# Kernel optimization log

Measured on AMD Instinct MI355X. Metric: run time of the kernel, lower is better.

## Reference

```python
import jax, jax.numpy as jnp
import numpy as np

N = 8192
D_IN = 512
HID = 1024
EMB = 64
N_EFF = 2
N_CLASSES = 16
MARGIN = 0.01


def setup_inputs() -> dict:
    key = jax.random.key(0)
    ks = jax.random.split(key, 10)
    data = jax.random.normal(ks[0], (N, D_IN), dtype=jnp.float32)
    labels = jax.random.randint(ks[1], (N,), 0, N_CLASSES).astype(jnp.float32)
    x = jnp.concatenate([labels[:, None], data], axis=1)  # [N, 1+D_IN]

    def lin(k, fan_in, fan_out):
        return jax.random.normal(k, (fan_in, fan_out), dtype=jnp.float32) / np.sqrt(fan_in)

    return {
        "x": x,
        "W1": lin(ks[2], D_IN, HID), "b1": jnp.zeros((HID,), jnp.float32),
        "W2": lin(ks[3], HID, EMB), "b2": jnp.zeros((EMB,), jnp.float32),
        "W3": lin(ks[4], EMB, HID), "b3": jnp.zeros((HID,), jnp.float32),
        "W4": lin(ks[5], HID, D_IN), "b4": jnp.zeros((D_IN,), jnp.float32),
    }


def reference(x, W1, b1, W2, b2, W3, b3, W4, b4):
    labels = x[:, 0]
    data = x[:, 1:]

    # encoder / decoder (tanh MLP autoencoder)
    embedding = jnp.tanh(data @ W1 + b1) @ W2 + b2          # [N, EMB]
    decoded = jnp.tanh(embedding @ W3 + b3) @ W4 + b4       # [N, D_IN]

    conserved = embedding[:, N_EFF:]                        # [N, C]
    n_conserved = conserved.shape[1]

    # labels.expand + unique(return_inverse) on row-replicated labels is
    # equivalent to comparing the labels directly.
    lbl = labels.astype(jnp.int32)
    Y = lbl[:, None] != lbl[None, :]                        # [N, N] bool

    # D_mean[i,j] = mean_d (c_i - c_j)^2, via Gram-matrix algebra (one pass,
    # no [N,N,C] intermediate).
    sq = jnp.sum(conserved * conserved, axis=1)             # [N]
    gram = conserved @ conserved.T                          # [N, N]
    D_mean = jnp.maximum(sq[:, None] + sq[None, :] - 2.0 * gram, 0.0) / n_conserved

    Yf = Y.astype(D_mean.dtype)
    n_diff = jnp.sum(Yf)
    C_sim = jnp.sum(Yf * D_mean) / (n_diff + 1.0)
    C_diff = jnp.sum((1.0 - Yf) * jnp.maximum(0.0, MARGIN - D_mean)) / (
        (D_mean.shape[0] * D_mean.shape[1] - n_diff) + 1.0)

    return decoded, C_sim, C_diff
```

## Files before the change

### kernel.cpp

```cpp
#include <hip/hip_runtime.h>
#include <stdint.h>

#define NROWS 8192
#define DIN   512
#define HIDN  1024
#define EMBN  64
#define NCONS 62
#define NCLS  16
#define MARGINF 0.01f
#define NREP  16

typedef unsigned short u16;
typedef __attribute__((ext_vector_type(8))) short short8;
typedef __attribute__((ext_vector_type(4))) float floatx4;

__device__ __forceinline__ u16 f32_to_bf16(float f) {
  union { float f; uint32_t u; } x; x.f = f;
  uint32_t u = x.u;
  uint32_t r = (u + 0x7FFFu + ((u >> 16) & 1u)) >> 16;
  return (u16)r;
}

__device__ __forceinline__ float bf16_to_f32(u16 h) {
  union { uint32_t u; float f; } x; x.u = (uint32_t)h << 16;
  return x.f;
}

__device__ __forceinline__ float fast_tanh(float x) {
  float xc = fminf(fmaxf(x, -10.f), 10.f);
  float e = __expf(2.f * xc);
  return (e - 1.f) * __builtin_amdgcn_rcpf(e + 1.f);
}

__device__ __forceinline__ void load_lds16(const u16* g, u16* l) {
  __builtin_amdgcn_global_load_lds(
      (const __attribute__((address_space(1))) void*)g,
      (__attribute__((address_space(3))) void*)l, 16, 0, 0);
}

__device__ __forceinline__ void pack_tile(const float* __restrict__ W,
                                          u16* __restrict__ Wp,
                                          int N, int KU, int t, int lane)
{
  const int r = lane >> 2, slot = lane & 3;
  const int c = slot ^ ((r >> 1) & 3);
  const int nt = t / KU, ku = t - nt * KU;
  const int n = nt * 16 + r;
  const int kb = ku * 32 + c * 8;
  short8 v;
#pragma unroll
  for (int j = 0; j < 8; ++j) v[j] = (short)f32_to_bf16(W[(size_t)(kb + j) * N + n]);
  *(short8*)(Wp + ((size_t)t * 64 + lane) * 8) = v;
}

__global__ __launch_bounds__(256)
void prep_all(const float* __restrict__ x,
              const float* __restrict__ W1, const float* __restrict__ W2,
              const float* __restrict__ W3, const float* __restrict__ W4,
              u16* __restrict__ A0p, u16* __restrict__ W1p,
              u16* __restrict__ W2p, u16* __restrict__ W3p,
              u16* __restrict__ W4p, float* __restrict__ slab,
              int* __restrict__ labels, int* __restrict__ hist32)
{
  __shared__ int hh[NCLS];
  const int b = blockIdx.x;
  const int tid = threadIdx.x;
  const int tl = tid >> 6, lane = tid & 63;
  if (b < 2048) {
    if (b < 32) {
      if (tid < NCLS) hh[tid] = 0;
      const int row = b * 256 + tid;
      const int lab = (int)x[(size_t)row * 513];
      labels[row] = lab;
      __syncthreads();
      atomicAdd(&hh[lab], 1);
      __syncthreads();
      if (tid < NCLS) hist32[b * NCLS + tid] = hh[tid];
    }
    const int t = b * 4 + tl;
    const int rt = t >> 4, ku = t & 15;
    const int r = lane & 15, q = lane >> 4;
    const float* src = x + (size_t)(rt * 16 + r) * 513 + 1 + ku * 32 + q * 8;
    short8 v;
#pragma unroll
    for (int j = 0; j < 8; ++j) v[j] = (short)f32_to_bf16(src[j]);
    *(short8*)(A0p + ((size_t)t * 64 + lane) * 8) = v;
  } else if (b < 2304) {
    pack_tile(W1, W1p, 1024, 16, (b - 2048) * 4 + tl, lane);
  } else if (b < 2336) {
    pack_tile(W2, W2p, 64, 32, (b - 2304) * 4 + tl, lane);
  } else if (b < 2368) {
    pack_tile(W3, W3p, 1024, 2, (b - 2336) * 4 + tl, lane);
  } else if (b < 2624) {
    pack_tile(W4, W4p, 512, 32, (b - 2368) * 4 + tl, lane);
  } else {
    float* dst = slab + (size_t)(b - 2624) * 4096;
    for (int i = tid; i < 4096; i += 256) dst[i] = 0.f;
  }
}

__global__ __launch_bounds__(256)
void gemm12(const u16* __restrict__ A0p, const u16* __restrict__ W1p,
            const float* __restrict__ b1, const u16* __restrict__ W2p,
            float* __restrict__ Ef4,
            const int* __restrict__ labels, const int* __restrict__ hist32,
            int* __restrict__ offs, int* __restrict__ counts,
            int* __restrict__ idx)
{
  __shared__ u16 lB[2][16 * 512];
  __shared__ u16 Hc[4][64 * 66];
  __shared__ int colsum[NCLS], preblk[NCLS], scur[NCLS];

  const int tid = threadIdx.x, wave = tid >> 6, lane = tid & 63;

  if (blockIdx.x >= 128) {
    const int sb = (blockIdx.x - 128) * 4 + blockIdx.y;
    if (tid < NCLS) {
      int s = 0, p = 0;
      for (int b2 = 0; b2 < 32; ++b2) {
        const int h = hist32[b2 * NCLS + tid];
        s += h;
        if (b2 < sb * 2) p += h;
      }
      colsum[tid] = s;
      preblk[tid] = p;
    }
    __syncthreads();
    if (tid < NCLS) {
      int o = 0;
      for (int c = 0; c < tid; ++c) o += colsum[c];
      scur[tid] = o + preblk[tid];
      if (sb == 0) {
        counts[tid] = colsum[tid];
        offs[tid] = o;
        if (tid == NCLS - 1) offs[NCLS] = o + colsum[NCLS - 1];
      }
    }
    __syncthreads();
    for (int i = tid; i < 512; i += 256) {
      const int row = sb * 512 + i;
      const int p = atomicAdd(&scur[labels[row]], 1);
      idx[p] = row;
    }
    return;
  }

  const int quad = lane >> 4, l15 = lane & 15;
  const int wm = wave >> 1, wn = wave & 1;
  const int xslot = (l15 >> 1) & 3;
  const int m0 = blockIdx.x * 64;
  const int g = blockIdx.y;

  floatx4 Hacc[4][2][2];
#pragma unroll
  for (int c = 0; c < 4; ++c)
#pragma unroll
    for (int i = 0; i < 2; ++i)
#pragma unroll
      for (int j = 0; j < 2; ++j) Hacc[c][i][j] = (floatx4){0.f, 0.f, 0.f, 0.f};

#pragma unroll
  for (int u = 0; u < 4; ++u) {
    const int jt = wave + u * 4;
    load_lds16(W1p + (size_t)((g * 16 + jt) * 16) * 512 + lane * 8, lB[0] + jt * 512);
  }
  __syncthreads();

  for (int s = 0; s < 16; ++s) {
    const int p = s & 1;
    if (s < 15) {
#pragma unroll
      for (int u = 0; u < 4; ++u) {
        const int jt = wave + u * 4;
        load_lds16(W1p + (size_t)((g * 16 + jt) * 16 + s + 1) * 512 + lane * 8,
                   lB[1 - p] + jt * 512);
      }
    }
    short8 af[2];
#pragma unroll
    for (int i = 0; i < 2; ++i)
      af[i] = *(const short8*)(A0p +
               (size_t)((blockIdx.x * 4 + wm * 2 + i) * 16 + s) * 512 + lane * 8);
#pragma unroll
    for (int c = 0; c < 4; ++c)
#pragma unroll
      for (int j = 0; j < 2; ++j) {
        const short8 bf = *(const short8*)(lB[p] + (c * 4 + wn * 2 + j) * 512
                              + l15 * 32 + ((quad ^ xslot) << 3));
#pragma unroll
        for (int i = 0; i < 2; ++i)
          Hacc[c][i][j] = __builtin_amdgcn_mfma_f32_16x16x32_bf16(af[i], bf, Hacc[c][i][j], 0, 0, 0);
      }
    __syncthreads();
  }

  u16* lW2 = &lB[0][0];
#pragma unroll
  for (int u = 0; u < 8; ++u) {
    const int t = wave * 8 + u;
    load_lds16(W2p + (size_t)((t >> 3) * 32 + g * 8 + (t & 7)) * 512 + lane * 8,
               lW2 + t * 512);
  }
#pragma unroll
  for (int c = 0; c < 4; ++c)
#pragma unroll
    for (int j = 0; j < 2; ++j) {
      const int col = wn * 32 + j * 16 + l15;
      const float bv = b1[g * 256 + c * 64 + col];
#pragma unroll
      for (int i = 0; i < 2; ++i)
#pragma unroll
        for (int r = 0; r < 4; ++r)
          Hc[c][(wm * 32 + i * 16 + quad * 4 + r) * 66 + col] =
              f32_to_bf16(fast_tanh(Hacc[c][i][j][r] + bv));
    }
  __syncthreads();

  floatx4 Eacc[2][2];
#pragma unroll
  for (int i = 0; i < 2; ++i)
#pragma unroll
    for (int j = 0; j < 2; ++j) Eacc[i][j] = (floatx4){0.f, 0.f, 0.f, 0.f};

#pragma unroll
  for (int es = 0; es < 8; ++es) {
    const int cc = es >> 1, hh2 = es & 1;
    short8 af2[2];
#pragma unroll
    for (int i = 0; i < 2; ++i)
      af2[i] = *(const short8*)(Hc[cc] + (wm * 32 + i * 16 + l15) * 66 + hh2 * 32 + quad * 8);
#pragma unroll
    for (int j = 0; j < 2; ++j) {
      const short8 bf = *(const short8*)(lW2 + ((wn * 2 + j) * 8 + es) * 512
                            + l15 * 32 + ((quad ^ xslot) << 3));
#pragma unroll
      for (int i = 0; i < 2; ++i)
        Eacc[i][j] = __builtin_amdgcn_mfma_f32_16x16x32_bf16(af2[i], bf, Eacc[i][j], 0, 0, 0);
    }
  }

  float* Efg = Ef4 + (size_t)g * NROWS * 64;
#pragma unroll
  for (int i = 0; i < 2; ++i)
#pragma unroll
    for (int j = 0; j < 2; ++j) {
      const int col = wn * 32 + j * 16 + l15;
#pragma unroll
      for (int r = 0; r < 4; ++r) {
        const int row = m0 + wm * 32 + i * 16 + quad * 4 + r;
        Efg[(size_t)row * 64 + col] = Eacc[i][j][r];
      }
    }
}

__global__ __launch_bounds__(256)
void stats3(const float* __restrict__ Ef4, const float* __restrict__ b2,
            const int* __restrict__ labels, const u16* __restrict__ W3p,
            const float* __restrict__ b3,
            u16* __restrict__ Ebf, float* __restrict__ sqrow,
            float* __restrict__ vsumR, float* __restrict__ SsumR,
            u16* __restrict__ T)
{
  __shared__ float lv[NCLS][64];
  __shared__ float lsq[NCLS][64];
  __shared__ u16 El[32 * 66];
  const int tid = threadIdx.x;
  for (int i = tid; i < NCLS * 64; i += 256) {
    ((float*)lv)[i] = 0.f; ((float*)lsq)[i] = 0.f;
  }
  __syncthreads();

  const int rep = blockIdx.x & (NREP - 1);
  const int wave = tid >> 6, lane = tid & 63;
  const float bv = b2[lane];
  const int base0 = blockIdx.x * 32;
  const int base = base0 + wave * 8;
  for (int r = 0; r < 8; ++r) {
    const int row = base + r;
    const int c = labels[row];
    float acc = bv;
#pragma unroll
    for (int g = 0; g < 4; ++g)
      acc += Ef4[((size_t)g * NROWS + row) * 64 + lane];
    const u16 h = f32_to_bf16(acc);
    Ebf[(size_t)row * 64 + lane] = h;
    El[(wave * 8 + r) * 66 + lane] = h;
    float v = bf16_to_f32(h);
    if (lane < 2) v = 0.f;
    const float v2 = v * v;
    atomicAdd(&lv[c][lane], v);
    atomicAdd(&lsq[c][lane], v2);
    float s = v2;
    for (int o = 32; o > 0; o >>= 1) s += __shfl_xor(s, o);
    if (lane == 0) sqrow[row] = s;
  }
  __syncthreads();

  for (int i = tid; i < NCLS * 64; i += 256) {
    const int c = i >> 6, k = i & 63;
    if (k >= 2) atomicAdd(&vsumR[rep * (NCLS * NCONS) + c * NCONS + k - 2], lv[c][k]);
  }
  if (tid < NCLS) {
    float s = 0.f;
    for (int k = 0; k < 64; ++k) s += lsq[tid][k];
    atomicAdd(&SsumR[rep * NCLS + tid], s);
  }

  const int quad = lane >> 4, l15 = lane & 15;
  const int wn = wave;
  const int lamb = l15 * 4 + (quad ^ ((l15 >> 1) & 3));

  floatx4 acc3[2][16];
#pragma unroll
  for (int i = 0; i < 2; ++i)
#pragma unroll
    for (int jj = 0; jj < 16; ++jj) acc3[i][jj] = (floatx4){0.f, 0.f, 0.f, 0.f};

#pragma unroll
  for (int kk = 0; kk < 2; ++kk) {
    short8 af[2];
#pragma unroll
    for (int i = 0; i < 2; ++i)
      af[i] = *(const short8*)(El + (i * 16 + l15) * 66 + kk * 32 + quad * 8);
#pragma unroll
    for (int jj = 0; jj < 16; ++jj) {
      const int nt = wn * 16 + jj;
      const short8 bf = *(const short8*)(W3p + (size_t)(nt * 2 + kk) * 512 + lamb * 8);
#pragma unroll
      for (int i = 0; i < 2; ++i)
        acc3[i][jj] = __builtin_amdgcn_mfma_f32_16x16x32_bf16(af[i], bf, acc3[i][jj], 0, 0, 0);
    }
  }

#pragma unroll
  for (int i = 0; i < 2; ++i)
#pragma unroll
    for (int jj = 0; jj < 16; ++jj) {
      const int col = wn * 256 + jj * 16 + l15;
      const float bv3 = b3[col];
#pragma unroll
      for (int r = 0; r < 4; ++r) {
        const int row = base0 + i * 16 + quad * 4 + r;
        T[(size_t)row * 1024 + col] = f32_to_bf16(fast_tanh(acc3[i][jj][r] + bv3));
      }
    }
}

__global__ __launch_bounds__(256)
void tail(const u16* __restrict__ T, const u16* __restrict__ W4p,
          const float* __restrict__ b4, float* __restrict__ out,
          const u16* __restrict__ Ebf, const float* __restrict__ sqrow,
          const int* __restrict__ idx, const int* __restrict__ offs,
          float* __restrict__ pair_sum)
{
  __shared__ u16 uni[24576];
  const int tid = threadIdx.x, wave = tid >> 6, lane = tid & 63;
  const int quad = lane >> 4, l15 = lane & 15;

  if (blockIdx.x < 512) {
    u16* lA = uni;
    u16* lBb = uni + 16384;
    const int wm = wave >> 1, wn = wave & 1;
    const int xslot = (l15 >> 1) & 3;
    const int lin = blockIdx.x;
    const int n0 = (lin >> 6) * 64;
    const int m0 = (lin & 63) * 128;
    const int srow = lane >> 2;
    const int schunk = (lane & 3) ^ ((lane >> 3) & 3);

    auto stage = [&](int s, int buf) {
#pragma unroll
      for (int q = 0; q < 6; ++q) {
        const int u = wave + q * 4;
        if (u < 16) {
          const int rg = u >> 1, kh = u & 1;
          load_lds16(T + (size_t)(m0 + rg * 16 + srow) * 1024 + s * 64 + kh * 32 + schunk * 8,
                     lA + buf * 8192 + u * 512 + lane * 8);
        } else {
          const int v = u - 16, nt = v >> 1, kh = v & 1;
          load_lds16(W4p + (size_t)(((n0 >> 4) + nt) * 32 + s * 2 + kh) * 512 + lane * 8,
                     lBb + buf * 4096 + v * 512 + lane * 8);
        }
      }
    };

    stage(0, 0);
    __syncthreads();

    floatx4 acc[4][2];
#pragma unroll
    for (int i = 0; i < 4; ++i)
#pragma unroll
      for (int j = 0; j < 2; ++j) acc[i][j] = (floatx4){0.f, 0.f, 0.f, 0.f};

    for (int s = 0; s < 16; ++s) {
      const int p = s & 1;
      if (s < 15) stage(s + 1, 1 - p);
#pragma unroll
      for (int kk = 0; kk < 2; ++kk) {
        short8 af[4], bf[2];
#pragma unroll
        for (int i = 0; i < 4; ++i)
          af[i] = *(const short8*)(lA + p * 8192 + ((wm * 4 + i) * 2 + kk) * 512
                                   + l15 * 32 + ((quad ^ xslot) << 3));
#pragma unroll
        for (int j = 0; j < 2; ++j)
          bf[j] = *(const short8*)(lBb + p * 4096 + ((wn * 2 + j) * 2 + kk) * 512
                                   + l15 * 32 + ((quad ^ xslot) << 3));
#pragma unroll
        for (int i = 0; i < 4; ++i)
#pragma unroll
          for (int j = 0; j < 2; ++j)
            acc[i][j] = __builtin_amdgcn_mfma_f32_16x16x32_bf16(af[i], bf[j], acc[i][j], 0, 0, 0);
      }
      __syncthreads();
    }

#pragma unroll
    for (int i = 0; i < 4; ++i)
#pragma unroll
      for (int j = 0; j < 2; ++j) {
        const int col = n0 + wn * 32 + j * 16 + l15;
        const float bv = b4[col];
#pragma unroll
        for (int r = 0; r < 4; ++r) {
          const int row = m0 + wm * 64 + i * 16 + quad * 4 + r;
          out[(size_t)row * 512 + col] = acc[i][j][r] + bv;
        }
      }
    return;
  }

  const int q = blockIdx.x - 512;
  const int cls = q / 21;
  int p = q - cls * 21, ti = 0, cnt = 6;
  while (p >= cnt) { p -= cnt; ++ti; --cnt; }
  const int tj = ti + p;

  const int start = offs[cls];
  const int n = offs[cls + 1] - start;
  if (ti * 128 >= n || tj * 128 >= n) return;

  constexpr int LDA = 66;
  u16* Li = uni;
  u16* Lj = uni + 128 * LDA;
  float* sqI = (float*)(uni + 2 * 128 * LDA);
  float* sqJ = sqI + 128;
  float* red4 = sqJ + 128;

  for (int e = tid; e < 2048; e += 256) {
    const int t = e >> 10;
    const int row = (e >> 3) & 127;
    const int ch = e & 7;
    const int g = (t ? tj : ti) * 128 + row;
    short8 v = (short8)0;
    if (g < n) {
      v = *(const short8*)(Ebf + (size_t)idx[start + g] * EMBN + ch * 8);
      if (ch == 0) { v[0] = 0; v[1] = 0; }
    }
    *(short8*)((t ? Lj : Li) + row * LDA + ch * 8) = v;
  }
  {
    const int t = tid >> 7, row = tid & 127;
    const int g = (t ? tj : ti) * 128 + row;
    (t ? sqJ : sqI)[row] = (g < n) ? sqrow[idx[start + g]] : 0.f;
  }
  __syncthreads();

  const int wm = wave >> 1, wn = wave & 1;

  floatx4 acc[4][4];
#pragma unroll
  for (int i = 0; i < 4; ++i)
#pragma unroll
    for (int j = 0; j < 4; ++j) acc[i][j] = (floatx4){0.f, 0.f, 0.f, 0.f};

#pragma unroll
  for (int ks = 0; ks < 2; ++ks) {
    short8 af[4], bf[4];
#pragma unroll
    for (int i = 0; i < 4; ++i)
      af[i] = *(const short8*)(Li + (wm * 64 + i * 16 + l15) * LDA + ks * 32 + quad * 8);
#pragma unroll
    for (int j = 0; j < 4; ++j)
      bf[j] = *(const short8*)(Lj + (wn * 64 + j * 16 + l15) * LDA + ks * 32 + quad * 8);
#pragma unroll
    for (int i = 0; i < 4; ++i)
#pragma unroll
      for (int j = 0; j < 4; ++j)
        acc[i][j] = __builtin_amdgcn_mfma_f32_16x16x32_bf16(af[i], bf[j], acc[i][j], 0, 0, 0);
  }

  float local = 0.f;
#pragma unroll
  for (int i = 0; i < 4; ++i)
#pragma unroll
    for (int j = 0; j < 4; ++j)
#pragma unroll
      for (int r = 0; r < 4; ++r) {
        const int row = wm * 64 + i * 16 + quad * 4 + r;
        const int col = wn * 64 + j * 16 + l15;
        const int gi = ti * 128 + row, gj = tj * 128 + col;
        if (gi < n && gj < n && gi != gj) {
          const float D = (sqI[row] + sqJ[col] - 2.f * acc[i][j][r]) * (1.f / 62.f);
          local += fmaxf(0.f, MARGINF - D);
        }
      }
  if (ti < tj) local *= 2.f;

  for (int o = 32; o > 0; o >>= 1) local += __shfl_xor(local, o);
  if (lane == 0) red4[wave] = local;
  __syncthreads();
  if (tid == 0)
    atomicAdd(pair_sum, red4[0] + red4[1] + red4[2] + red4[3]);
}

__device__ __forceinline__ double block_reduce_d(double v, double* red, int tid) {
  red[tid] = v;
  __syncthreads();
  for (int st = 128; st > 0; st >>= 1) {
    if (tid < st) red[tid] += red[tid + st];
    __syncthreads();
  }
  const double r = red[0];
  __syncthreads();
  return r;
}

__global__ __launch_bounds__(256)
void finalize(const float* __restrict__ vsumR, const float* __restrict__ SsumR,
              const int* __restrict__ counts, const float* __restrict__ pair_sum,
              float* __restrict__ out2)
{
  const int tid = threadIdx.x;
  __shared__ double red[256];
  __shared__ float vtot[NCLS * NCONS];

  for (int i = tid; i < NCLS * NCONS; i += 256) {
    float s = 0.f;
    for (int r = 0; r < NREP; ++r) s += vsumR[r * (NCLS * NCONS) + i];
    vtot[i] = s;
  }
  __syncthreads();

  double v = 0.0;
  if (tid < NCLS) {
    float Sc = 0.f;
    for (int r = 0; r < NREP; ++r) Sc += SsumR[r * NCLS + tid];
    v = (double)Sc * (double)(NROWS - counts[tid]);
  }
  const double t1 = block_reduce_d(v, red, tid);

  v = 0.0;
  if (tid < NCLS) { const double nc = (double)counts[tid]; v = nc * nc; }
  const double n_same = block_reduce_d(v, red, tid);

  v = 0.0;
  for (int i = tid; i < NCLS * NCONS; i += 256) { const double w = vtot[i]; v += w * w; }
  const double t2 = block_reduce_d(v, red, tid);

  v = 0.0;
  if (tid < NCONS) {
    double Vk = 0.0;
    for (int c = 0; c < NCLS; ++c) Vk += (double)vtot[c * NCONS + tid];
    v = Vk * Vk;
  }
  const double t3 = block_reduce_d(v, red, tid);

  if (tid == 0) {
    const double n_diff = (double)NROWS * (double)NROWS - n_same;
    const double sim = 2.0 * t1 - 2.0 * (t3 - t2);
    const double C_sim = sim / 62.0 / (n_diff + 1.0);
    const double C_diff = ((double)pair_sum[0] + (double)NROWS * (double)MARGINF)
                          / (n_same + 1.0);
    out2[0] = (float)C_sim;
    out2[1] = (float)C_diff;
  }
}

extern "C" void kernel_launch(void* const* d_in, const int* in_sizes, int n_in,
                              void* d_out, int out_size, void* d_ws, size_t ws_size,
                              hipStream_t stream)
{
  const float* x  = (const float*)d_in[0];
  const float* W1 = (const float*)d_in[1];
  const float* b1 = (const float*)d_in[2];
  const float* W2 = (const float*)d_in[3];
  const float* b2 = (const float*)d_in[4];
  const float* W3 = (const float*)d_in[5];
  const float* b3 = (const float*)d_in[6];
  const float* W4 = (const float*)d_in[7];
  const float* b4 = (const float*)d_in[8];
  float* out = (float*)d_out;

  char* ws = (char*)d_ws;
  const size_t KB = 1024, MB = 1ull << 20;
  u16* A0p    = (u16*)(ws + 0);
  u16* W1p    = (u16*)(ws + 8 * MB);
  u16* W2p    = (u16*)(ws + 9 * MB);
  u16* W3p    = (u16*)(ws + 9 * MB + 128 * KB);
  u16* W4p    = (u16*)(ws + 9 * MB + 256 * KB);
  float* Ef4  = (float*)(ws + 10 * MB + 256 * KB);
  u16* Ebf    = (u16*)(ws + 18 * MB + 256 * KB);
  int* labels = (int*)(ws + 19 * MB + 256 * KB);
  int* idx    = (int*)(ws + 19 * MB + 288 * KB);
  float* sqrow = (float*)(ws + 19 * MB + 320 * KB);
  int* hist32 = (int*)(ws + 19 * MB + 352 * KB);
  float* slab = (float*)(ws + 19 * MB + 384 * KB);
  int*   counts  = (int*)slab;
  int*   offs    = counts + 16;
  float* psum    = slab + 64;
  float* SsumR   = slab + 128;
  float* vsumR   = slab + 512;
  u16* T      = (u16*)(ws + 20 * MB);
  (void)in_sizes; (void)n_in; (void)out_size; (void)ws_size;

  prep_all<<<dim3(2630), dim3(256), 0, stream>>>(x, W1, W2, W3, W4,
                                                 A0p, W1p, W2p, W3p, W4p,
                                                 slab, labels, hist32);
  gemm12<<<dim3(132, 4), dim3(256), 0, stream>>>(A0p, W1p, b1, W2p, Ef4,
                                                 labels, hist32, offs, counts, idx);
  stats3<<<dim3(256), dim3(256), 0, stream>>>(Ef4, b2, labels, W3p, b3,
                                              Ebf, sqrow, vsumR, SsumR, T);
  tail<<<dim3(848), dim3(256), 0, stream>>>(T, W4p, b4, out,
                                            Ebf, sqrow, idx, offs, psum);
  finalize<<<dim3(1), dim3(256), 0, stream>>>(vsumR, SsumR, counts, psum,
                                              out + (size_t)NROWS * DIN);
}
```

Before: 172.2 us.

## Fuse encoder GEMMs, embedding stats and W3 layer into one kernel

Merges the gemm12 and stats3 kernels into a single 512-thread kernel. Each block now owns 32 full rows across all 1024 hidden units, so the embedding is reduced in shared memory rather than written as four fp32 partial slabs to global memory and read back. W1/W2 tiles are read straight from global memory instead of being double-buffered through LDS, and the grid drops from 132x4 to 272 blocks. This removes a launch and the Ef4 global round trip, but each block repeats W1 loads from cache, and the larger LDS footprint with fewer blocks may lower occupancy.

New measurement: 174.7 us. No clear change (+1.4%).

```diff
diff --git a/kernel.cpp b/kernel.cpp
--- a/kernel.cpp
+++ b/kernel.cpp
@@ -99,28 +99,34 @@
   }
 }
 
-__global__ __launch_bounds__(256)
-void gemm12(const u16* __restrict__ A0p, const u16* __restrict__ W1p,
-            const float* __restrict__ b1, const u16* __restrict__ W2p,
-            float* __restrict__ Ef4,
-            const int* __restrict__ labels, const int* __restrict__ hist32,
-            int* __restrict__ offs, int* __restrict__ counts,
-            int* __restrict__ idx)
+__global__ __launch_bounds__(512)
+void fused123(const u16* __restrict__ A0p, const u16* __restrict__ W1p,
+              const float* __restrict__ b1, const u16* __restrict__ W2p,
+              const float* __restrict__ b2, const u16* __restrict__ W3p,
+              const float* __restrict__ b3,
+              const int* __restrict__ labels, const int* __restrict__ hist32,
+              int* __restrict__ offs, int* __restrict__ counts,
+              int* __restrict__ idx,
+              u16* __restrict__ Ebf, float* __restrict__ sqrow,
+              float* __restrict__ vsumR, float* __restrict__ SsumR,
+              u16* __restrict__ T)
 {
-  __shared__ u16 lB[2][16 * 512];
-  __shared__ u16 Hc[4][64 * 66];
+  __shared__ u16 uni[33024];
+  __shared__ u16 El[32 * 66];
+  __shared__ float lv[NCLS][64];
+  __shared__ float lsq[NCLS][64];
   __shared__ int colsum[NCLS], preblk[NCLS], scur[NCLS];
 
-  const int tid = threadIdx.x, wave = tid >> 6, lane = tid & 63;
-
-  if (blockIdx.x >= 128) {
-    const int sb = (blockIdx.x - 128) * 4 + blockIdx.y;
+  const int tid = threadIdx.x;
+
+  if (blockIdx.x < 16) {
+    const int sb = blockIdx.x;
     if (tid < NCLS) {
       int s = 0, p = 0;
-      for (int b2 = 0; b2 < 32; ++b2) {
-        const int h = hist32[b2 * NCLS + tid];
+      for (int b2i = 0; b2i < 32; ++b2i) {
+        const int h = hist32[b2i * NCLS + tid];
         s += h;
-        if (b2 < sb * 2) p += h;
+        if (b2i < sb * 2) p += h;
       }
       colsum[tid] = s;
       preblk[tid] = p;
@@ -137,166 +143,117 @@
       }
     }
     __syncthreads();
-    for (int i = tid; i < 512; i += 256) {
-      const int row = sb * 512 + i;
+    {
+      const int row = sb * 512 + tid;
       const int p = atomicAdd(&scur[labels[row]], 1);
       idx[p] = row;
     }
     return;
   }
 
+  const int bx = blockIdx.x - 16;
+  const int m0 = bx * 32;
+  const int rep = blockIdx.x & (NREP - 1);
+  const int w = tid >> 6, lane = tid & 63;
   const int quad = lane >> 4, l15 = lane & 15;
-  const int wm = wave >> 1, wn = wave & 1;
-  const int xslot = (l15 >> 1) & 3;
-  const int m0 = blockIdx.x * 64;
-  const int g = blockIdx.y;
-
-  floatx4 Hacc[4][2][2];
-#pragma unroll
-  for (int c = 0; c < 4; ++c)
+  const int lamb = l15 * 4 + (quad ^ ((l15 >> 1) & 3));
+
+  for (int i = tid; i < NCLS * 64; i += 512) {
+    ((float*)lv)[i] = 0.f; ((float*)lsq)[i] = 0.f;
+  }
+
+  u16* Hc = uni;
+  float* Epart = (float*)uni;
+
+  floatx4 acc1[2][8];
+#pragma unroll
+  for (int i = 0; i < 2; ++i)
+#pragma unroll
+    for (int jj = 0; jj < 8; ++jj) acc1[i][jj] = (floatx4){0.f, 0.f, 0.f, 0.f};
+
+  for (int s = 0; s < 16; ++s) {
+    short8 af[2];
 #pragma unroll
     for (int i = 0; i < 2; ++i)
-#pragma unroll
-      for (int j = 0; j < 2; ++j) Hacc[c][i][j] = (floatx4){0.f, 0.f, 0.f, 0.f};
-
-#pragma unroll
-  for (int u = 0; u < 4; ++u) {
-    const int jt = wave + u * 4;
-    load_lds16(W1p + (size_t)((g * 16 + jt) * 16) * 512 + lane * 8, lB[0] + jt * 512);
-  }
-  __syncthreads();
-
-  for (int s = 0; s < 16; ++s) {
-    const int p = s & 1;
-    if (s < 15) {
-#pragma unroll
-      for (int u = 0; u < 4; ++u) {
-        const int jt = wave + u * 4;
-        load_lds16(W1p + (size_t)((g * 16 + jt) * 16 + s + 1) * 512 + lane * 8,
-                   lB[1 - p] + jt * 512);
-      }
-    }
+      af[i] = *(const short8*)(A0p + (size_t)((bx * 2 + i) * 16 + s) * 512 + lane * 8);
+#pragma unroll
+    for (int jj = 0; jj < 8; ++jj) {
+      const short8 bf = *(const short8*)(W1p + (size_t)((w * 8 + jj) * 16 + s) * 512 + lamb * 8);
+#pragma unroll
+      for (int i = 0; i < 2; ++i)
+        acc1[i][jj] = __builtin_amdgcn_mfma_f32_16x16x32_bf16(af[i], bf, acc1[i][jj], 0, 0, 0);
+    }
+  }
+#pragma unroll
+  for (int jj = 0; jj < 8; ++jj) {
+    const int col = w * 128 + jj * 16 + l15;
+    const float bv = b1[col];
+#pragma unroll
+    for (int i = 0; i < 2; ++i)
+#pragma unroll
+      for (int r = 0; r < 4; ++r)
+        Hc[(i * 16 + quad * 4 + r) * 1032 + col] = f32_to_bf16(fast_tanh(acc1[i][jj][r] + bv));
+  }
+  __syncthreads();
+
+  floatx4 acc2[2][4];
+#pragma unroll
+  for (int i = 0; i < 2; ++i)
+#pragma unroll
+    for (int nt = 0; nt < 4; ++nt) acc2[i][nt] = (floatx4){0.f, 0.f, 0.f, 0.f};
+
+#pragma unroll
+  for (int kk = 0; kk < 4; ++kk) {
+    const int ku = w * 4 + kk;
     short8 af[2];
 #pragma unroll
     for (int i = 0; i < 2; ++i)
-      af[i] = *(const short8*)(A0p +
-               (size_t)((blockIdx.x * 4 + wm * 2 + i) * 16 + s) * 512 + lane * 8);
-#pragma unroll
-    for (int c = 0; c < 4; ++c)
-#pragma unroll
-      for (int j = 0; j < 2; ++j) {
-        const short8 bf = *(const short8*)(lB[p] + (c * 4 + wn * 2 + j) * 512
-                              + l15 * 32 + ((quad ^ xslot) << 3));
-#pragma unroll
-        for (int i = 0; i < 2; ++i)
-          Hacc[c][i][j] = __builtin_amdgcn_mfma_f32_16x16x32_bf16(af[i], bf, Hacc[c][i][j], 0, 0, 0);
-      }
-    __syncthreads();
-  }
-
-  u16* lW2 = &lB[0][0];
-#pragma unroll
-  for (int u = 0; u < 8; ++u) {
-    const int t = wave * 8 + u;
-    load_lds16(W2p + (size_t)((t >> 3) * 32 + g * 8 + (t & 7)) * 512 + lane * 8,
-               lW2 + t * 512);
-  }
-#pragma unroll
-  for (int c = 0; c < 4; ++c)
-#pragma unroll
-    for (int j = 0; j < 2; ++j) {
-      const int col = wn * 32 + j * 16 + l15;
-      const float bv = b1[g * 256 + c * 64 + col];
+      af[i] = *(const short8*)(Hc + (i * 16 + l15) * 1032 + ku * 32 + quad * 8);
+#pragma unroll
+    for (int nt = 0; nt < 4; ++nt) {
+      const short8 bf = *(const short8*)(W2p + (size_t)(nt * 32 + ku) * 512 + lamb * 8);
 #pragma unroll
       for (int i = 0; i < 2; ++i)
-#pragma unroll
-        for (int r = 0; r < 4; ++r)
-          Hc[c][(wm * 32 + i * 16 + quad * 4 + r) * 66 + col] =
-              f32_to_bf16(fast_tanh(Hacc[c][i][j][r] + bv));
-    }
-  __syncthreads();
-
-  floatx4 Eacc[2][2];
+        acc2[i][nt] = __builtin_amdgcn_mfma_f32_16x16x32_bf16(af[i], bf, acc2[i][nt], 0, 0, 0);
+    }
+  }
+  __syncthreads();
+
 #pragma unroll
   for (int i = 0; i < 2; ++i)
 #pragma unroll
-    for (int j = 0; j < 2; ++j) Eacc[i][j] = (floatx4){0.f, 0.f, 0.f, 0.f};
-
-#pragma unroll
-  for (int es = 0; es < 8; ++es) {
-    const int cc = es >> 1, hh2 = es & 1;
-    short8 af2[2];
-#pragma unroll
-    for (int i = 0; i < 2; ++i)
-      af2[i] = *(const short8*)(Hc[cc] + (wm * 32 + i * 16 + l15) * 66 + hh2 * 32 + quad * 8);
-#pragma unroll
-    for (int j = 0; j < 2; ++j) {
-      const short8 bf = *(const short8*)(lW2 + ((wn * 2 + j) * 8 + es) * 512
-                            + l15 * 32 + ((quad ^ xslot) << 3));
-#pragma unroll
-      for (int i = 0; i < 2; ++i)
-        Eacc[i][j] = __builtin_amdgcn_mfma_f32_16x16x32_bf16(af2[i], bf, Eacc[i][j], 0, 0, 0);
-    }
-  }
-
-  float* Efg = Ef4 + (size_t)g * NROWS * 64;
-#pragma unroll
-  for (int i = 0; i < 2; ++i)
-#pragma unroll
-    for (int j = 0; j < 2; ++j) {
-      const int col = wn * 32 + j * 16 + l15;
-#pragma unroll
-      for (int r = 0; r < 4; ++r) {
-        const int row = m0 + wm * 32 + i * 16 + quad * 4 + r;
-        Efg[(size_t)row * 64 + col] = Eacc[i][j][r];
-      }
-    }
-}
-
-__global__ __launch_bounds__(256)
-void stats3(const float* __restrict__ Ef4, const float* __restrict__ b2,
-            const int* __restrict__ labels, const u16* __restrict__ W3p,
-            const float* __restrict__ b3,
-            u16* __restrict__ Ebf, float* __restrict__ sqrow,
-            float* __restrict__ vsumR, float* __restrict__ SsumR,
-            u16* __restrict__ T)
-{
-  __shared__ float lv[NCLS][64];
-  __shared__ float lsq[NCLS][64];
-  __shared__ u16 El[32 * 66];
-  const int tid = threadIdx.x;
-  for (int i = tid; i < NCLS * 64; i += 256) {
-    ((float*)lv)[i] = 0.f; ((float*)lsq)[i] = 0.f;
-  }
-  __syncthreads();
-
-  const int rep = blockIdx.x & (NREP - 1);
-  const int wave = tid >> 6, lane = tid & 63;
-  const float bv = b2[lane];
-  const int base0 = blockIdx.x * 32;
-  const int base = base0 + wave * 8;
-  for (int r = 0; r < 8; ++r) {
-    const int row = base + r;
-    const int c = labels[row];
-    float acc = bv;
-#pragma unroll
-    for (int g = 0; g < 4; ++g)
-      acc += Ef4[((size_t)g * NROWS + row) * 64 + lane];
-    const u16 h = f32_to_bf16(acc);
-    Ebf[(size_t)row * 64 + lane] = h;
-    El[(wave * 8 + r) * 66 + lane] = h;
-    float v = bf16_to_f32(h);
-    if (lane < 2) v = 0.f;
-    const float v2 = v * v;
-    atomicAdd(&lv[c][lane], v);
-    atomicAdd(&lsq[c][lane], v2);
-    float s = v2;
-    for (int o = 32; o > 0; o >>= 1) s += __shfl_xor(s, o);
-    if (lane == 0) sqrow[row] = s;
-  }
-  __syncthreads();
-
-  for (int i = tid; i < NCLS * 64; i += 256) {
+    for (int nt = 0; nt < 4; ++nt)
+#pragma unroll
+      for (int r = 0; r < 4; ++r)
+        Epart[((size_t)w * 32 + i * 16 + quad * 4 + r) * 64 + nt * 16 + l15] = acc2[i][nt][r];
+  __syncthreads();
+
+  if (w < 4) {
+    const float bv2 = b2[lane];
+    for (int r = 0; r < 8; ++r) {
+      const int row = w * 8 + r;
+      const int grow = m0 + row;
+      const int c = labels[grow];
+      float acc = bv2;
+#pragma unroll
+      for (int p = 0; p < 8; ++p)
+        acc += Epart[((size_t)p * 32 + row) * 64 + lane];
+      const u16 h = f32_to_bf16(acc);
+      Ebf[(size_t)grow * 64 + lane] = h;
+      El[row * 66 + lane] = h;
+      float v = bf16_to_f32(h);
+      if (lane < 2) v = 0.f;
+      const float v2 = v * v;
+      atomicAdd(&lv[c][lane], v);
+      atomicAdd(&lsq[c][lane], v2);
+      float s = v2;
+      for (int o = 32; o > 0; o >>= 1) s += __shfl_xor(s, o);
+      if (lane == 0) sqrow[grow] = s;
+    }
+  }
+  __syncthreads();
+
+  for (int i = tid; i < NCLS * 64; i += 512) {
     const int c = i >> 6, k = i & 63;
     if (k >= 2) atomicAdd(&vsumR[rep * (NCLS * NCONS) + c * NCONS + k - 2], lv[c][k]);
   }
@@ -306,15 +263,11 @@
     atomicAdd(&SsumR[rep * NCLS + tid], s);
   }
 
-  const int quad = lane >> 4, l15 = lane & 15;
-  const int wn = wave;
-  const int lamb = l15 * 4 + (quad ^ ((l15 >> 1) & 3));
-
-  floatx4 acc3[2][16];
+  floatx4 acc3[2][8];
 #pragma unroll
   for (int i = 0; i < 2; ++i)
 #pragma unroll
-    for (int jj = 0; jj < 16; ++jj) acc3[i][jj] = (floatx4){0.f, 0.f, 0.f, 0.f};
+    for (int jj = 0; jj < 8; ++jj) acc3[i][jj] = (floatx4){0.f, 0.f, 0.f, 0.f};
 
 #pragma unroll
   for (int kk = 0; kk < 2; ++kk) {
@@ -323,27 +276,25 @@
     for (int i = 0; i < 2; ++i)
       af[i] = *(const short8*)(El + (i * 16 + l15) * 66 + kk * 32 + quad * 8);
 #pragma unroll
-    for (int jj = 0; jj < 16; ++jj) {
-      const int nt = wn * 16 + jj;
+    for (int jj = 0; jj < 8; ++jj) {
+      const int nt = w * 8 + jj;
       const short8 bf = *(const short8*)(W3p + (size_t)(nt * 2 + kk) * 512 + lamb * 8);
 #pragma unroll
       for (int i = 0; i < 2; ++i)
         acc3[i][jj] = __builtin_amdgcn_mfma_f32_16x16x32_bf16(af[i], bf, acc3[i][jj], 0, 0, 0);
     }
   }
-
-#pragma unroll
-  for (int i = 0; i < 2; ++i)
-#pragma unroll
-    for (int jj = 0; jj < 16; ++jj) {
-      const int col = wn * 256 + jj * 16 + l15;
-      const float bv3 = b3[col];
-#pragma unroll
-      for (int r = 0; r < 4; ++r) {
-        const int row = base0 + i * 16 + quad * 4 + r;
-        T[(size_t)row * 1024 + col] = f32_to_bf16(fast_tanh(acc3[i][jj][r] + bv3));
-      }
-    }
+#pragma unroll
+  for (int jj = 0; jj < 8; ++jj) {
+    const int col = w * 128 + jj * 16 + l15;
+    const float bv3 = b3[col];
+#pragma unroll
+    for (int i = 0; i < 2; ++i)
+#pragma unroll
+      for (int r = 0; r < 4; ++r)
+        T[(size_t)(m0 + i * 16 + quad * 4 + r) * 1024 + col] =
+            f32_to_bf16(fast_tanh(acc3[i][jj][r] + bv3));
+  }
 }
 
 __global__ __launch_bounds__(256)
@@ -600,7 +551,6 @@
   u16* W2p    = (u16*)(ws + 9 * MB);
   u16* W3p    = (u16*)(ws + 9 * MB + 128 * KB);
   u16* W4p    = (u16*)(ws + 9 * MB + 256 * KB);
-  float* Ef4  = (float*)(ws + 10 * MB + 256 * KB);
   u16* Ebf    = (u16*)(ws + 18 * MB + 256 * KB);
   int* labels = (int*)(ws + 19 * MB + 256 * KB);
   int* idx    = (int*)(ws + 19 * MB + 288 * KB);
@@ -618,10 +568,9 @@
   prep_all<<<dim3(2630), dim3(256), 0, stream>>>(x, W1, W2, W3, W4,
                                                  A0p, W1p, W2p, W3p, W4p,
                                                  slab, labels, hist32);
-  gemm12<<<dim3(132, 4), dim3(256), 0, stream>>>(A0p, W1p, b1, W2p, Ef4,
-                                                 labels, hist32, offs, counts, idx);
-  stats3<<<dim3(256), dim3(256), 0, stream>>>(Ef4, b2, labels, W3p, b3,
-                                              Ebf, sqrow, vsumR, SsumR, T);
+  fused123<<<dim3(272), dim3(512), 0, stream>>>(A0p, W1p, b1, W2p, b2, W3p, b3,
+                                                labels, hist32, offs, counts, idx,
+                                                Ebf, sqrow, vsumR, SsumR, T);
   tail<<<dim3(848), dim3(256), 0, stream>>>(T, W4p, b4, out,
                                             Ebf, sqrow, idx, offs, psum);
   finalize<<<dim3(1), dim3(256), 0, stream>>>(vsumR, SsumR, counts, psum,
```
